# Optimization experiments

Measured on AMD Instinct MI355X. Metric: run time of the kernel, lower is better.

## Reference

```python
import jax, jax.numpy as jnp
import numpy as np

DIM = 64
HEADS = 8
WIN = (8, 8)  # window_num


def setup_inputs() -> dict:
    key = jax.random.key(0)
    ks = jax.random.split(key, 6)
    b, c, H, W = 16, DIM, 256, 256
    n = WIN[0] * WIN[1]
    x = jax.random.normal(ks[0], (b, c, H, W), dtype=jnp.float32)
    w_qkv = jax.random.normal(ks[1], (3 * c, c), dtype=jnp.float32) * (1.0 / np.sqrt(c))
    w_dw = jax.random.normal(ks[2], (3 * c, 1, 3, 3), dtype=jnp.float32) * (1.0 / 3.0)
    w_proj = jax.random.normal(ks[3], (c, c), dtype=jnp.float32) * (1.0 / np.sqrt(c))
    b_proj = jnp.zeros((c,), dtype=jnp.float32)
    # trunc_normal_(std=1) approximated by clipped normal for the reference baseline
    pos_emb = jnp.clip(jax.random.normal(ks[4], (1, HEADS, n, n), dtype=jnp.float32), -2.0, 2.0)
    return {"x": x, "w_qkv": w_qkv, "w_dw": w_dw, "w_proj": w_proj,
            "b_proj": b_proj, "pos_emb": pos_emb}


def _to_window_tokens(t, n0, n1, heads):
    # t: [b, c, n0*b0, n1*b1] -> [b, heads, n0*n1, (b0*b1*c)//heads]
    b, c, H, W = t.shape
    b0, b1 = H // n0, W // n1
    t = t.reshape(b, c, n0, b0, n1, b1)
    t = t.transpose(0, 2, 4, 3, 5, 1)            # b n0 n1 b0 b1 c
    t = t.reshape(b, n0 * n1, b0 * b1 * c)       # b n (b0 b1 c)
    d = (b0 * b1 * c) // heads
    return t.reshape(b, n0 * n1, heads, d).transpose(0, 2, 1, 3)  # b h n d


def _from_window_tokens(t, n0, n1, b0, b1, c):
    # t: [b, heads, n, d] -> [b, c, n0*b0, n1*b1]
    b = t.shape[0]
    t = t.transpose(0, 2, 1, 3).reshape(b, n0 * n1, b0 * b1 * c)  # b n (h d)
    t = t.reshape(b, n0, n1, b0, b1, c)
    t = t.transpose(0, 5, 1, 3, 2, 4)            # b c n0 b0 n1 b1
    return t.reshape(b, c, n0 * b0, n1 * b1)


def reference(x, w_qkv, w_dw, w_proj, b_proj, pos_emb):
    b, c, H, W = x.shape
    n0, n1 = WIN
    b0, b1 = H // n0, W // n1
    # 1x1 pointwise qkv projection (no bias)
    qkv = jnp.einsum('bchw,oc->bohw', x, w_qkv)
    # 3x3 depthwise conv, padding=1, groups=3c, no bias
    qkv = jax.lax.conv_general_dilated(
        qkv, w_dw, window_strides=(1, 1), padding=((1, 1), (1, 1)),
        feature_group_count=3 * c,
        dimension_numbers=('NCHW', 'OIHW', 'NCHW'))
    q, k, v = jnp.split(qkv, 3, axis=1)
    q = _to_window_tokens(q, n0, n1, HEADS)
    k = _to_window_tokens(k, n0, n1, HEADS)
    v = _to_window_tokens(v, n0, n1, HEADS)
    head_dim = b0 * b1 * c / HEADS
    scale = head_dim ** (-0.5)
    sim = jnp.einsum('bhid,bhjd->bhij', q * scale, k) + pos_emb
    attn = jax.nn.softmax(sim, axis=-1)
    out = jnp.einsum('bhij,bhjd->bhid', attn, v)
    out = _from_window_tokens(out, n0, n1, b0, b1, c)
    # 1x1 projection with bias
    out = jnp.einsum('bchw,oc->bohw', out, w_proj) + b_proj[None, :, None, None]
    return out
```

## Files before the change

### kernel.cpp

```cpp
#include <hip/hip_runtime.h>
#include <hip/hip_bf16.h>

typedef __hip_bfloat16 bf16;
typedef unsigned int u32;
typedef __attribute__((ext_vector_type(8))) short bf16x8;
typedef __attribute__((ext_vector_type(4))) float f32x4;

#define HWSZ 65536u

__device__ __forceinline__ float b2f_lo(u32 w){ return __uint_as_float(w << 16); }
__device__ __forceinline__ float b2f_hi(u32 w){ return __uint_as_float(w & 0xffff0000u); }
__device__ __forceinline__ float b2f(bf16 v){ return __bfloat162float(v); }
__device__ __forceinline__ bf16 f2b(float v){ return __float2bfloat16(v); }

__device__ __forceinline__ u32 f2bbits(float f){
  u32 x = __float_as_uint(f);
  return ((x + 0x7fffu + ((x >> 16) & 1u)) >> 16) & 0xffffu;
}

__device__ __forceinline__ void unpack8(uint4 v, float* f){
  f[0]=b2f_lo(v.x); f[1]=b2f_hi(v.x);
  f[2]=b2f_lo(v.y); f[3]=b2f_hi(v.y);
  f[4]=b2f_lo(v.z); f[5]=b2f_hi(v.z);
  f[6]=b2f_lo(v.w); f[7]=b2f_hi(v.w);
}

union ABu { u32 u[4]; bf16x8 v; uint4 q; };

__global__ __launch_bounds__(256) void k12_fused(
    const float* __restrict__ x, const float* __restrict__ wq,
    const float* __restrict__ wdw, bf16* __restrict__ tok){
  __shared__ uint4 xs[8 * 192];
  __shared__ unsigned short qs[192 * 68];
  int t = threadIdx.x;
  int lane = t & 63, w = t >> 6;
  int r16 = lane & 15, g4 = lane >> 4;

  u32 n = blockIdx.x;
  u32 bid = (n & 7u) * 1024u + (n >> 3);
  u32 xt = bid & 31u, yt = (bid >> 5) & 15u, b = bid >> 9;
  int y0 = (int)yt * 16, x0 = (int)xt * 8;

  const float* xb = x + (size_t)b * 64 * HWSZ;

  bf16x8 af[3][2];
  #pragma unroll
  for (int g = 0; g < 3; g++){
    int och = g * 64 + w * 16 + r16;
    #pragma unroll
    for (int kt = 0; kt < 2; kt++){
      const float* wr = wq + och * 64 + kt * 32 + g4 * 8;
      ABu pk;
      #pragma unroll
      for (int j = 0; j < 4; j++)
        pk.u[j] = f2bbits(wr[2 * j]) | (f2bbits(wr[2 * j + 1]) << 16);
      af[g][kt] = pk.v;
    }
  }

  for (int u = t; u < 288; u += 256){
    int jh = u & 1, rr = (u >> 1) % 18, c8 = u / 36;
    int yy = y0 - 1 + rr;
    float va[4][10];
    if ((u32)yy < 256u){
      #pragma unroll
      for (int jc = 0; jc < 4; jc++){
        const float* p = xb + (size_t)(c8 * 8 + jh * 4 + jc) * HWSZ + ((size_t)yy << 8);
        float4 A  = *(const float4*)(p + x0);
        float4 Bq = *(const float4*)(p + x0 + 4);
        va[jc][0] = (x0 > 0) ? p[x0 - 1] : 0.f;
        va[jc][1] = A.x;  va[jc][2] = A.y;  va[jc][3] = A.z;  va[jc][4] = A.w;
        va[jc][5] = Bq.x; va[jc][6] = Bq.y; va[jc][7] = Bq.z; va[jc][8] = Bq.w;
        va[jc][9] = (x0 + 8 < 256) ? p[x0 + 8] : 0.f;
      }
    } else {
      #pragma unroll
      for (int jc = 0; jc < 4; jc++)
        #pragma unroll
        for (int e = 0; e < 10; e++) va[jc][e] = 0.f;
    }
    #pragma unroll
    for (int e = 0; e < 10; e++){
      u32 w0 = f2bbits(va[0][e]) | (f2bbits(va[1][e]) << 16);
      u32 w1 = f2bbits(va[2][e]) | (f2bbits(va[3][e]) << 16);
      int a16 = c8 * 192 + rr * 10 + e;
      a16 = (a16 & ~7) | ((a16 ^ (a16 >> 3)) & 7);
      ((uint2*)&xs[a16])[jh] = make_uint2(w0, w1);
    }
  }
  if (t < 96){
    int c8 = t / 12, px = 180 + (t % 12);
    int a16 = c8 * 192 + px;
    a16 = (a16 & ~7) | ((a16 ^ (a16 >> 3)) & 7);
    xs[a16] = make_uint4(0u, 0u, 0u, 0u);
  }

  int cth = t & 63, rq = w;
  int h = (int)(yt & 1u) * 4 + rq;
  u32 win = (yt >> 1) * 8u + (xt >> 2);

  for (int g = 0; g < 3; g++){
    __syncthreads();
    #pragma unroll
    for (int nt = 0; nt < 12; nt++){
      f32x4 acc = (f32x4){0.f, 0.f, 0.f, 0.f};
      #pragma unroll
      for (int kt = 0; kt < 2; kt++){
        int a16 = (kt * 4 + g4) * 192 + nt * 16 + r16;
        a16 = (a16 & ~7) | ((a16 ^ (a16 >> 3)) & 7);
        uint4 uq = xs[a16];
        acc = __builtin_amdgcn_mfma_f32_16x16x32_bf16(
            af[g][kt], *reinterpret_cast<bf16x8*>(&uq), acc, 0, 0, 0);
      }
      int px = nt * 16 + r16;
      u32 lo = f2bbits(acc[0]) | (f2bbits(acc[1]) << 16);
      u32 hi = f2bbits(acc[2]) | (f2bbits(acc[3]) << 16);
      *(uint2*)&qs[px * 68 + w * 16 + g4 * 4] = make_uint2(lo, hi);
    }
    __syncthreads();

    const float* wg = wdw + ((size_t)g * 64 + cth) * 9;
    float d0=wg[0],d1=wg[1],d2=wg[2],d3=wg[3],d4=wg[4],d5=wg[5],d6=wg[6],d7=wg[7],d8=wg[8];
    bf16* op = tok + (((((size_t)g * 16 + b) * 8 + h) * 64 + win) * 8192)
             + (size_t)(xt & 3u) * 512 + cth;
    float rbf[3][10];
    #define QLD(s, R) do{ _Pragma("unroll") for (int _cr = 0; _cr < 10; _cr++) \
      rbf[s][_cr] = __uint_as_float(((u32)qs[((R) * 10 + _cr) * 68 + cth]) << 16); }while(0)
    QLD(0, rq * 4 + 0);
    QLD(1, rq * 4 + 1);
    QLD(2, rq * 4 + 2);
    #pragma unroll
    for (int rr2 = 0; rr2 < 4; rr2++){
      const int sT = rr2 % 3, sM = (rr2 + 1) % 3, sB = (rr2 + 2) % 3;
      #pragma unroll
      for (int co = 0; co < 8; co++){
        float o = rbf[sT][co]*d0 + rbf[sT][co+1]*d1 + rbf[sT][co+2]*d2
                + rbf[sM][co]*d3 + rbf[sM][co+1]*d4 + rbf[sM][co+2]*d5
                + rbf[sB][co]*d6 + rbf[sB][co+1]*d7 + rbf[sB][co+2]*d8;
        op[(size_t)rr2 * 2048 + co * 64] = f2b(o);
      }
      if (rr2 < 3) QLD(sT, rq * 4 + rr2 + 3);
    }
    #undef QLD
  }
}

__global__ __launch_bounds__(256) void k3_sim(
    const bf16* __restrict__ tok, float* __restrict__ sim4){
  __shared__ short qs[64 * 72];
  __shared__ short ks[64 * 72];
  int t = threadIdx.x;
  int lane = t & 63, w = t >> 6;
  int r16 = lane & 15, g4 = lane >> 4;
  u32 bid = blockIdx.x;
  u32 part = bid & 3u, h = (bid >> 2) & 7u, b = bid >> 5;
  const bf16* qb = tok + ((size_t)(((0 * 16 + b) * 8 + h) * 64)) * 8192 + part * 2048;
  const bf16* kb = tok + ((size_t)(((1 * 16 + b) * 8 + h) * 64)) * 8192 + part * 2048;

  int stok = t >> 2, soct = t & 3;

  f32x4 acc[4];
  #pragma unroll
  for (int jt = 0; jt < 4; jt++) acc[jt] = (f32x4){0.f,0.f,0.f,0.f};

  for (int s = 0; s < 32; s++){
    int d0 = s * 64;
    __syncthreads();
    {
      uint4 q0 = *(const uint4*)(qb + (size_t)stok * 8192 + d0 + soct * 8);
      uint4 q1 = *(const uint4*)(qb + (size_t)stok * 8192 + d0 + soct * 8 + 32);
      uint4 k0 = *(const uint4*)(kb + (size_t)stok * 8192 + d0 + soct * 8);
      uint4 k1 = *(const uint4*)(kb + (size_t)stok * 8192 + d0 + soct * 8 + 32);
      *(uint4*)&qs[stok * 72 + soct * 8]      = q0;
      *(uint4*)&qs[stok * 72 + soct * 8 + 32] = q1;
      *(uint4*)&ks[stok * 72 + soct * 8]      = k0;
      *(uint4*)&ks[stok * 72 + soct * 8 + 32] = k1;
    }
    __syncthreads();
    #pragma unroll
    for (int kt = 0; kt < 2; kt++){
      bf16x8 a = *(const bf16x8*)&qs[(w * 16 + r16) * 72 + kt * 32 + g4 * 8];
      #pragma unroll
      for (int jt = 0; jt < 4; jt++){
        bf16x8 bb = *(const bf16x8*)&ks[(jt * 16 + r16) * 72 + kt * 32 + g4 * 8];
        acc[jt] = __builtin_amdgcn_mfma_f32_16x16x32_bf16(a, bb, acc[jt], 0, 0, 0);
      }
    }
  }

  float* sp = sim4 + ((((size_t)part * 16 + b) * 8 + h) * 64) * 64;
  #pragma unroll
  for (int jt = 0; jt < 4; jt++)
    #pragma unroll
    for (int r = 0; r < 4; r++)
      sp[(w * 16 + g4 * 4 + r) * 64 + jt * 16 + r16] = acc[jt][r];
}

__global__ __launch_bounds__(64) void k4_softmax(
    const float* __restrict__ sim4, const float* __restrict__ pos, float* __restrict__ attn){
  int j = threadIdx.x;
  u32 bid = blockIdx.x;
  u32 i = bid & 63u, h = (bid >> 6) & 7u, b = bid >> 9;
  size_t o = (((size_t)b * 8 + h) * 64 + i) * 64 + j;
  const size_t pstride = (size_t)16 * 8 * 64 * 64;
  float s = sim4[o] + sim4[o + pstride] + sim4[o + 2 * pstride] + sim4[o + 3 * pstride];
  s = s * 0.011048543456039806f + pos[(((size_t)h * 64) + i) * 64 + j];
  float m = s;
  #pragma unroll
  for (int off = 32; off; off >>= 1) m = fmaxf(m, __shfl_xor(m, off));
  float e = __expf(s - m);
  float sum = e;
  #pragma unroll
  for (int off = 32; off; off >>= 1) sum += __shfl_xor(sum, off);
  attn[o] = e / sum;
}

__global__ __launch_bounds__(256) void k5_av(
    const bf16* __restrict__ tok, const float* __restrict__ attn, bf16* __restrict__ otok){
  __shared__ short vt[4][64 * 72];
  int t = threadIdx.x;
  int lane = t & 63, w = t >> 6;
  int r16 = lane & 15, g4 = lane >> 4;
  u32 bid = blockIdx.x;
  u32 q = bid & 3u, h = (bid >> 2) & 7u, b = bid >> 5;
  const bf16* vb = tok + ((size_t)(((2 * 16 + b) * 8 + h) * 64)) * 8192;
  const float* ab = attn + (((size_t)b * 8 + h) * 64) * 64;
  bf16* ob = otok + (((size_t)b * 8 + h) * 64) * 8192;

  bf16x8 af[4][2];
  #pragma unroll
  for (int it = 0; it < 4; it++)
    #pragma unroll
    for (int kt = 0; kt < 2; kt++){
      const float* ar = ab + (it * 16 + r16) * 64 + kt * 32 + g4 * 8;
      ABu pk;
      #pragma unroll
      for (int j = 0; j < 4; j++)
        pk.u[j] = f2bbits(ar[2 * j]) | (f2bbits(ar[2 * j + 1]) << 16);
      af[it][kt] = pk.v;
    }

  short* vtw = vt[w];
  for (int s = 0; s < 8; s++){
    int d0 = (int)q * 2048 + s * 256 + w * 64;
    uint4 ld[8];
    const bf16* vp = vb + (size_t)lane * 8192 + d0;
    #pragma unroll
    for (int u = 0; u < 8; u++) ld[u] = *(const uint4*)(vp + u * 8);
    #pragma unroll
    for (int u = 0; u < 8; u++){
      const u32* wd = (const u32*)&ld[u];
      #pragma unroll
      for (int e = 0; e < 4; e++){
        int d = u * 8 + e * 2;
        vtw[d * 72 + lane]       = (short)(wd[e] & 0xffffu);
        vtw[(d + 1) * 72 + lane] = (short)(wd[e] >> 16);
      }
    }
    #pragma unroll
    for (int dt = 0; dt < 4; dt++){
      bf16x8 b0 = *(const bf16x8*)&vtw[(dt * 16 + r16) * 72 + 0 * 32 + g4 * 8];
      bf16x8 b1 = *(const bf16x8*)&vtw[(dt * 16 + r16) * 72 + 1 * 32 + g4 * 8];
      #pragma unroll
      for (int it = 0; it < 4; it++){
        f32x4 acc = (f32x4){0.f,0.f,0.f,0.f};
        acc = __builtin_amdgcn_mfma_f32_16x16x32_bf16(af[it][0], b0, acc, 0, 0, 0);
        acc = __builtin_amdgcn_mfma_f32_16x16x32_bf16(af[it][1], b1, acc, 0, 0, 0);
        #pragma unroll
        for (int r = 0; r < 4; r++)
          ob[(size_t)(it * 16 + g4 * 4 + r) * 8192 + d0 + dt * 16 + r16] = f2b(acc[r]);
      }
    }
  }
}

__global__ __launch_bounds__(256) void k6_mfma(
    const bf16* __restrict__ otok, const float* __restrict__ wp,
    const float* __restrict__ bp, float* __restrict__ out){
  __shared__ uint4 xs[1024];
  int t = threadIdx.x;
  int lane = t & 63, w = t >> 6;
  u32 pix0 = blockIdx.x * 128u;
  u32 b = pix0 >> 16, hw0 = pix0 & 65535u;
  int y = (int)(hw0 >> 8);
  int p0 = y & 31, h = p0 >> 2, prow = (p0 & 3) * 2048;
  int iy = (y >> 5) << 3;

  {
    int pix = t & 127, half = t >> 7;
    int xx = (int)(hw0 & 255u) + pix;
    int i = iy + (xx >> 5), p1 = xx & 31;
    const bf16* ip = otok + ((((size_t)b * 8 + h) * 64 + i)) * 8192 + prow + p1 * 64;
    #pragma unroll
    for (int g = 0; g < 4; g++){
      int c8 = half * 4 + g;
      xs[c8 * 128 + pix] = *(const uint4*)(ip + c8 * 8);
    }
  }

  int r16 = lane & 15, g4 = lane >> 4;
  bf16x8 af[2];
  int och = w * 16 + r16;
  #pragma unroll
  for (int kt = 0; kt < 2; kt++){
    const float* wr = wp + och * 64 + kt * 32 + g4 * 8;
    ABu pk;
    #pragma unroll
    for (int j = 0; j < 4; j++)
      pk.u[j] = f2bbits(wr[2 * j]) | (f2bbits(wr[2 * j + 1]) << 16);
    af[kt] = pk.v;
  }
  float bias[4];
  #pragma unroll
  for (int r = 0; r < 4; r++) bias[r] = bp[w * 16 + g4 * 4 + r];
  __syncthreads();

  f32x4 acc[8];
  #pragma unroll
  for (int pt = 0; pt < 8; pt++) acc[pt] = (f32x4){bias[0], bias[1], bias[2], bias[3]};

  #pragma unroll
  for (int pt = 0; pt < 8; pt++){
    uint4 u0 = xs[(0 * 4 + g4) * 128 + pt * 16 + r16];
    uint4 u1 = xs[(1 * 4 + g4) * 128 + pt * 16 + r16];
    bf16x8 b0 = *reinterpret_cast<bf16x8*>(&u0);
    bf16x8 b1 = *reinterpret_cast<bf16x8*>(&u1);
    acc[pt] = __builtin_amdgcn_mfma_f32_16x16x32_bf16(af[0], b0, acc[pt], 0, 0, 0);
    acc[pt] = __builtin_amdgcn_mfma_f32_16x16x32_bf16(af[1], b1, acc[pt], 0, 0, 0);
  }

  float* op = out + (size_t)b * 64 * HWSZ + hw0;
  int ochb = w * 16 + g4 * 4;
  #pragma unroll
  for (int pt = 0; pt < 8; pt++)
    #pragma unroll
    for (int r = 0; r < 4; r++)
      op[(size_t)(ochb + r) * HWSZ + pt * 16 + r16] = acc[pt][r];
}

extern "C" void kernel_launch(void* const* d_in, const int* in_sizes, int n_in,
                              void* d_out, int out_size, void* d_ws, size_t ws_size,
                              hipStream_t stream){
  const float* x   = (const float*)d_in[0];
  const float* wq  = (const float*)d_in[1];
  const float* wdw = (const float*)d_in[2];
  const float* wp  = (const float*)d_in[3];
  const float* bp  = (const float*)d_in[4];
  const float* pos = (const float*)d_in[5];
  float* out = (float*)d_out;
  (void)in_sizes; (void)n_in; (void)out_size; (void)ws_size;

  char* ws = (char*)d_ws;
  bf16*  tok  = (bf16*)(ws + 402653184u);
  bf16*  otok = (bf16*)ws;
  float* sim4 = (float*)(ws + 134217728u);
  float* attn = (float*)(ws + 142606336u);

  k12_fused<<<dim3(8192), dim3(256), 0, stream>>>(x, wq, wdw, tok);
  k3_sim<<<dim3(512),   dim3(256), 0, stream>>>(tok, sim4);
  k4_softmax<<<dim3(8192), dim3(64), 0, stream>>>(sim4, pos, attn);
  k5_av<<<dim3(512),  dim3(256), 0, stream>>>(tok, attn, otok);
  k6_mfma<<<dim3(8192), dim3(256), 0, stream>>>(otok, wp, bp, out);
}
```

Before: 524.7 us.

## Double k12 block to 512 threads and split work across more waves

The fused qkv-projection plus depthwise-conv kernel now runs 512 threads per block instead of 256. Each wave handles half the MFMA pixel tiles and two output rows instead of four, and the staging load is spread over more threads. Weight fragments are loaded per group inside the loop instead of all up front, which lowers register pressure so that launch_bounds(512,6) can be met. The aim is more latency hiding and occupancy, at the cost of redundant weight loads and extra halo row reads in the depthwise stage.

```diff
diff --git a/kernel.cpp b/kernel.cpp
--- a/kernel.cpp
+++ b/kernel.cpp
@@ -27,7 +27,11 @@
 
 union ABu { u32 u[4]; bf16x8 v; uint4 q; };
 
-__global__ __launch_bounds__(256) void k12_fused(
+__device__ __forceinline__ int xsw(int c8, int px){
+  return c8 * 192 + ((px & ~7) | ((px ^ c8) & 7));
+}
+
+__global__ __launch_bounds__(512, 6) void k12_fused(
     const float* __restrict__ x, const float* __restrict__ wq,
     const float* __restrict__ wdw, bf16* __restrict__ tok){
   __shared__ uint4 xs[8 * 192];
@@ -43,29 +47,14 @@
 
   const float* xb = x + (size_t)b * 64 * HWSZ;
 
-  bf16x8 af[3][2];
-  #pragma unroll
-  for (int g = 0; g < 3; g++){
-    int och = g * 64 + w * 16 + r16;
-    #pragma unroll
-    for (int kt = 0; kt < 2; kt++){
-      const float* wr = wq + och * 64 + kt * 32 + g4 * 8;
-      ABu pk;
-      #pragma unroll
-      for (int j = 0; j < 4; j++)
-        pk.u[j] = f2bbits(wr[2 * j]) | (f2bbits(wr[2 * j + 1]) << 16);
-      af[g][kt] = pk.v;
-    }
-  }
-
-  for (int u = t; u < 288; u += 256){
-    int jh = u & 1, rr = (u >> 1) % 18, c8 = u / 36;
+  for (int u = t; u < 576; u += 512){
+    int jq = u & 3, rr = (u >> 2) % 18, c8 = u / 72;
     int yy = y0 - 1 + rr;
-    float va[4][10];
+    float va[2][10];
     if ((u32)yy < 256u){
       #pragma unroll
-      for (int jc = 0; jc < 4; jc++){
-        const float* p = xb + (size_t)(c8 * 8 + jh * 4 + jc) * HWSZ + ((size_t)yy << 8);
+      for (int jc = 0; jc < 2; jc++){
+        const float* p = xb + (size_t)(c8 * 8 + jq * 2 + jc) * HWSZ + ((size_t)yy << 8);
         float4 A  = *(const float4*)(p + x0);
         float4 Bq = *(const float4*)(p + x0 + 4);
         va[jc][0] = (x0 > 0) ? p[x0 - 1] : 0.f;
@@ -75,73 +64,81 @@
       }
     } else {
       #pragma unroll
-      for (int jc = 0; jc < 4; jc++)
+      for (int jc = 0; jc < 2; jc++)
         #pragma unroll
         for (int e = 0; e < 10; e++) va[jc][e] = 0.f;
     }
     #pragma unroll
     for (int e = 0; e < 10; e++){
-      u32 w0 = f2bbits(va[0][e]) | (f2bbits(va[1][e]) << 16);
-      u32 w1 = f2bbits(va[2][e]) | (f2bbits(va[3][e]) << 16);
-      int a16 = c8 * 192 + rr * 10 + e;
-      a16 = (a16 & ~7) | ((a16 ^ (a16 >> 3)) & 7);
-      ((uint2*)&xs[a16])[jh] = make_uint2(w0, w1);
+      u32 wv = f2bbits(va[0][e]) | (f2bbits(va[1][e]) << 16);
+      ((u32*)&xs[xsw(c8, rr * 10 + e)])[jq] = wv;
     }
   }
   if (t < 96){
     int c8 = t / 12, px = 180 + (t % 12);
-    int a16 = c8 * 192 + px;
-    a16 = (a16 & ~7) | ((a16 ^ (a16 >> 3)) & 7);
-    xs[a16] = make_uint4(0u, 0u, 0u, 0u);
-  }
-
-  int cth = t & 63, rq = w;
-  int h = (int)(yt & 1u) * 4 + rq;
+    xs[xsw(c8, px)] = make_uint4(0u, 0u, 0u, 0u);
+  }
+
+  int cth = lane, rp = w;
+  int ot = w & 3, nh = w >> 2;
   u32 win = (yt >> 1) * 8u + (xt >> 2);
 
   for (int g = 0; g < 3; g++){
     __syncthreads();
-    #pragma unroll
-    for (int nt = 0; nt < 12; nt++){
+    bf16x8 af[2];
+    {
+      int och = g * 64 + ot * 16 + r16;
+      #pragma unroll
+      for (int kt = 0; kt < 2; kt++){
+        const float* wr = wq + och * 64 + kt * 32 + g4 * 8;
+        ABu pk;
+        #pragma unroll
+        for (int j = 0; j < 4; j++)
+          pk.u[j] = f2bbits(wr[2 * j]) | (f2bbits(wr[2 * j + 1]) << 16);
+        af[kt] = pk.v;
+      }
+    }
+    #pragma unroll
+    for (int nt2 = 0; nt2 < 6; nt2++){
+      int nt = nh * 6 + nt2;
       f32x4 acc = (f32x4){0.f, 0.f, 0.f, 0.f};
       #pragma unroll
       for (int kt = 0; kt < 2; kt++){
-        int a16 = (kt * 4 + g4) * 192 + nt * 16 + r16;
-        a16 = (a16 & ~7) | ((a16 ^ (a16 >> 3)) & 7);
-        uint4 uq = xs[a16];
+        uint4 uq = xs[xsw(kt * 4 + g4, nt * 16 + r16)];
         acc = __builtin_amdgcn_mfma_f32_16x16x32_bf16(
-            af[g][kt], *reinterpret_cast<bf16x8*>(&uq), acc, 0, 0, 0);
+            af[kt], *reinterpret_cast<bf16x8*>(&uq), acc, 0, 0, 0);
       }
       int px = nt * 16 + r16;
       u32 lo = f2bbits(acc[0]) | (f2bbits(acc[1]) << 16);
       u32 hi = f2bbits(acc[2]) | (f2bbits(acc[3]) << 16);
-      *(uint2*)&qs[px * 68 + w * 16 + g4 * 4] = make_uint2(lo, hi);
+      *(uint2*)&qs[px * 68 + ot * 16 + g4 * 4] = make_uint2(lo, hi);
     }
     __syncthreads();
 
     const float* wg = wdw + ((size_t)g * 64 + cth) * 9;
     float d0=wg[0],d1=wg[1],d2=wg[2],d3=wg[3],d4=wg[4],d5=wg[5],d6=wg[6],d7=wg[7],d8=wg[8];
-    bf16* op = tok + (((((size_t)g * 16 + b) * 8 + h) * 64 + win) * 8192)
-             + (size_t)(xt & 3u) * 512 + cth;
-    float rbf[3][10];
+    float rbf[4][10];
     #define QLD(s, R) do{ _Pragma("unroll") for (int _cr = 0; _cr < 10; _cr++) \
       rbf[s][_cr] = __uint_as_float(((u32)qs[((R) * 10 + _cr) * 68 + cth]) << 16); }while(0)
-    QLD(0, rq * 4 + 0);
-    QLD(1, rq * 4 + 1);
-    QLD(2, rq * 4 + 2);
-    #pragma unroll
-    for (int rr2 = 0; rr2 < 4; rr2++){
-      const int sT = rr2 % 3, sM = (rr2 + 1) % 3, sB = (rr2 + 2) % 3;
+    QLD(0, rp * 2 + 0);
+    QLD(1, rp * 2 + 1);
+    QLD(2, rp * 2 + 2);
+    QLD(3, rp * 2 + 3);
+    #undef QLD
+    #pragma unroll
+    for (int rr2 = 0; rr2 < 2; rr2++){
+      int r = rp * 2 + rr2;
+      int h = (int)(yt & 1u) * 4 + (r >> 2);
+      bf16* op = tok + (((((size_t)g * 16 + b) * 8 + h) * 64 + win) * 8192)
+               + (size_t)(r & 3) * 2048 + (size_t)(xt & 3u) * 512 + cth;
       #pragma unroll
       for (int co = 0; co < 8; co++){
-        float o = rbf[sT][co]*d0 + rbf[sT][co+1]*d1 + rbf[sT][co+2]*d2
-                + rbf[sM][co]*d3 + rbf[sM][co+1]*d4 + rbf[sM][co+2]*d5
-                + rbf[sB][co]*d6 + rbf[sB][co+1]*d7 + rbf[sB][co+2]*d8;
-        op[(size_t)rr2 * 2048 + co * 64] = f2b(o);
-      }
-      if (rr2 < 3) QLD(sT, rq * 4 + rr2 + 3);
-    }
-    #undef QLD
+        float o = rbf[rr2][co]    * d0 + rbf[rr2][co + 1]    * d1 + rbf[rr2][co + 2]    * d2
+                + rbf[rr2 + 1][co]* d3 + rbf[rr2 + 1][co + 1]* d4 + rbf[rr2 + 1][co + 2]* d5
+                + rbf[rr2 + 2][co]* d6 + rbf[rr2 + 2][co + 1]* d7 + rbf[rr2 + 2][co + 2]* d8;
+        op[co * 64] = f2b(o);
+      }
+    }
   }
 }
 
@@ -356,7 +353,7 @@
   float* sim4 = (float*)(ws + 134217728u);
   float* attn = (float*)(ws + 142606336u);
 
-  k12_fused<<<dim3(8192), dim3(256), 0, stream>>>(x, wq, wdw, tok);
+  k12_fused<<<dim3(8192), dim3(512), 0, stream>>>(x, wq, wdw, tok);
   k3_sim<<<dim3(512),   dim3(256), 0, stream>>>(tok, sim4);
   k4_softmax<<<dim3(8192), dim3(64), 0, stream>>>(sim4, pos, attn);
   k5_av<<<dim3(512),  dim3(256), 0, stream>>>(tok, attn, otok);
```

Measured after the change: 549.6 us. 4.7% more time.

## Fuse softmax into attention-value kernel and swizzle LDS with channel group

Applied to the files above, without the earlier changes.

Removes the standalone softmax kernel. The AV kernel now reads the four partial sim buffers and the positional bias, then does the row softmax in registers with cross-lane shuffles before packing bf16 MFMA operands. This saves one launch and the attn round trip through global memory. Each of the 4 q-blocks per (b,h) now recomputes the same softmax, which is redundant work. Separately, the k12 LDS swizzle now XORs in the channel-group index to cut bank conflicts, and the qkv weight fragments are loaded per group to lower register pressure.

```diff
diff --git a/kernel.cpp b/kernel.cpp
--- a/kernel.cpp
+++ b/kernel.cpp
@@ -18,14 +18,11 @@
   return ((x + 0x7fffu + ((x >> 16) & 1u)) >> 16) & 0xffffu;
 }
 
-__device__ __forceinline__ void unpack8(uint4 v, float* f){
-  f[0]=b2f_lo(v.x); f[1]=b2f_hi(v.x);
-  f[2]=b2f_lo(v.y); f[3]=b2f_hi(v.y);
-  f[4]=b2f_lo(v.z); f[5]=b2f_hi(v.z);
-  f[6]=b2f_lo(v.w); f[7]=b2f_hi(v.w);
-}
-
 union ABu { u32 u[4]; bf16x8 v; uint4 q; };
+
+__device__ __forceinline__ int xsw(int c8, int px){
+  return c8 * 192 + ((px & ~7) | ((px ^ (px >> 3) ^ c8) & 7));
+}
 
 __global__ __launch_bounds__(256) void k12_fused(
     const float* __restrict__ x, const float* __restrict__ wq,
@@ -43,21 +40,6 @@
 
   const float* xb = x + (size_t)b * 64 * HWSZ;
 
-  bf16x8 af[3][2];
-  #pragma unroll
-  for (int g = 0; g < 3; g++){
-    int och = g * 64 + w * 16 + r16;
-    #pragma unroll
-    for (int kt = 0; kt < 2; kt++){
-      const float* wr = wq + och * 64 + kt * 32 + g4 * 8;
-      ABu pk;
-      #pragma unroll
-      for (int j = 0; j < 4; j++)
-        pk.u[j] = f2bbits(wr[2 * j]) | (f2bbits(wr[2 * j + 1]) << 16);
-      af[g][kt] = pk.v;
-    }
-  }
-
   for (int u = t; u < 288; u += 256){
     int jh = u & 1, rr = (u >> 1) % 18, c8 = u / 36;
     int yy = y0 - 1 + rr;
@@ -83,16 +65,12 @@
     for (int e = 0; e < 10; e++){
       u32 w0 = f2bbits(va[0][e]) | (f2bbits(va[1][e]) << 16);
       u32 w1 = f2bbits(va[2][e]) | (f2bbits(va[3][e]) << 16);
-      int a16 = c8 * 192 + rr * 10 + e;
-      a16 = (a16 & ~7) | ((a16 ^ (a16 >> 3)) & 7);
-      ((uint2*)&xs[a16])[jh] = make_uint2(w0, w1);
+      ((uint2*)&xs[xsw(c8, rr * 10 + e)])[jh] = make_uint2(w0, w1);
     }
   }
   if (t < 96){
     int c8 = t / 12, px = 180 + (t % 12);
-    int a16 = c8 * 192 + px;
-    a16 = (a16 & ~7) | ((a16 ^ (a16 >> 3)) & 7);
-    xs[a16] = make_uint4(0u, 0u, 0u, 0u);
+    xs[xsw(c8, px)] = make_uint4(0u, 0u, 0u, 0u);
   }
 
   int cth = t & 63, rq = w;
@@ -101,16 +79,27 @@
 
   for (int g = 0; g < 3; g++){
     __syncthreads();
+    bf16x8 af[2];
+    {
+      int och = g * 64 + w * 16 + r16;
+      #pragma unroll
+      for (int kt = 0; kt < 2; kt++){
+        const float* wr = wq + och * 64 + kt * 32 + g4 * 8;
+        ABu pk;
+        #pragma unroll
+        for (int j = 0; j < 4; j++)
+          pk.u[j] = f2bbits(wr[2 * j]) | (f2bbits(wr[2 * j + 1]) << 16);
+        af[kt] = pk.v;
+      }
+    }
     #pragma unroll
     for (int nt = 0; nt < 12; nt++){
       f32x4 acc = (f32x4){0.f, 0.f, 0.f, 0.f};
       #pragma unroll
       for (int kt = 0; kt < 2; kt++){
-        int a16 = (kt * 4 + g4) * 192 + nt * 16 + r16;
-        a16 = (a16 & ~7) | ((a16 ^ (a16 >> 3)) & 7);
-        uint4 uq = xs[a16];
+        uint4 uq = xs[xsw(kt * 4 + g4, nt * 16 + r16)];
         acc = __builtin_amdgcn_mfma_f32_16x16x32_bf16(
-            af[g][kt], *reinterpret_cast<bf16x8*>(&uq), acc, 0, 0, 0);
+            af[kt], *reinterpret_cast<bf16x8*>(&uq), acc, 0, 0, 0);
       }
       int px = nt * 16 + r16;
       u32 lo = f2bbits(acc[0]) | (f2bbits(acc[1]) << 16);
@@ -196,27 +185,9 @@
       sp[(w * 16 + g4 * 4 + r) * 64 + jt * 16 + r16] = acc[jt][r];
 }
 
-__global__ __launch_bounds__(64) void k4_softmax(
-    const float* __restrict__ sim4, const float* __restrict__ pos, float* __restrict__ attn){
-  int j = threadIdx.x;
-  u32 bid = blockIdx.x;
-  u32 i = bid & 63u, h = (bid >> 6) & 7u, b = bid >> 9;
-  size_t o = (((size_t)b * 8 + h) * 64 + i) * 64 + j;
-  const size_t pstride = (size_t)16 * 8 * 64 * 64;
-  float s = sim4[o] + sim4[o + pstride] + sim4[o + 2 * pstride] + sim4[o + 3 * pstride];
-  s = s * 0.011048543456039806f + pos[(((size_t)h * 64) + i) * 64 + j];
-  float m = s;
-  #pragma unroll
-  for (int off = 32; off; off >>= 1) m = fmaxf(m, __shfl_xor(m, off));
-  float e = __expf(s - m);
-  float sum = e;
-  #pragma unroll
-  for (int off = 32; off; off >>= 1) sum += __shfl_xor(sum, off);
-  attn[o] = e / sum;
-}
-
 __global__ __launch_bounds__(256) void k5_av(
-    const bf16* __restrict__ tok, const float* __restrict__ attn, bf16* __restrict__ otok){
+    const bf16* __restrict__ tok, const float* __restrict__ sim4,
+    const float* __restrict__ pos, bf16* __restrict__ otok){
   __shared__ short vt[4][64 * 72];
   int t = threadIdx.x;
   int lane = t & 63, w = t >> 6;
@@ -224,21 +195,59 @@
   u32 bid = blockIdx.x;
   u32 q = bid & 3u, h = (bid >> 2) & 7u, b = bid >> 5;
   const bf16* vb = tok + ((size_t)(((2 * 16 + b) * 8 + h) * 64)) * 8192;
-  const float* ab = attn + (((size_t)b * 8 + h) * 64) * 64;
   bf16* ob = otok + (((size_t)b * 8 + h) * 64) * 8192;
 
+  const float* s0 = sim4 + (((size_t)b * 8 + h) * 64) * 64;
+  const size_t pstr = (size_t)16 * 8 * 64 * 64;
+  const float* pb = pos + ((size_t)h * 64) * 64;
+  const float SC = 0.011048543456039806f;
+
   bf16x8 af[4][2];
   #pragma unroll
-  for (int it = 0; it < 4; it++)
+  for (int it = 0; it < 4; it++){
+    int row = it * 16 + r16;
+    const float* rp = s0 + (size_t)row * 64;
+    float ev[2][8];
     #pragma unroll
     for (int kt = 0; kt < 2; kt++){
-      const float* ar = ab + (it * 16 + r16) * 64 + kt * 32 + g4 * 8;
+      int jb = kt * 32 + g4 * 8;
+      #pragma unroll
+      for (int hq = 0; hq < 2; hq++){
+        float4 a0 = *(const float4*)(rp + jb + hq * 4);
+        float4 a1 = *(const float4*)(rp + pstr + jb + hq * 4);
+        float4 a2 = *(const float4*)(rp + 2 * pstr + jb + hq * 4);
+        float4 a3 = *(const float4*)(rp + 3 * pstr + jb + hq * 4);
+        float4 pe = *(const float4*)(pb + (size_t)row * 64 + jb + hq * 4);
+        ev[kt][hq * 4 + 0] = (a0.x + a1.x + a2.x + a3.x) * SC + pe.x;
+        ev[kt][hq * 4 + 1] = (a0.y + a1.y + a2.y + a3.y) * SC + pe.y;
+        ev[kt][hq * 4 + 2] = (a0.z + a1.z + a2.z + a3.z) * SC + pe.z;
+        ev[kt][hq * 4 + 3] = (a0.w + a1.w + a2.w + a3.w) * SC + pe.w;
+      }
+    }
+    float m = ev[0][0];
+    #pragma unroll
+    for (int kt = 0; kt < 2; kt++)
+      #pragma unroll
+      for (int j = 0; j < 8; j++) m = fmaxf(m, ev[kt][j]);
+    m = fmaxf(m, __shfl_xor(m, 16));
+    m = fmaxf(m, __shfl_xor(m, 32));
+    float sum = 0.f;
+    #pragma unroll
+    for (int kt = 0; kt < 2; kt++)
+      #pragma unroll
+      for (int j = 0; j < 8; j++){ ev[kt][j] = __expf(ev[kt][j] - m); sum += ev[kt][j]; }
+    sum += __shfl_xor(sum, 16);
+    sum += __shfl_xor(sum, 32);
+    float inv = 1.f / sum;
+    #pragma unroll
+    for (int kt = 0; kt < 2; kt++){
       ABu pk;
       #pragma unroll
       for (int j = 0; j < 4; j++)
-        pk.u[j] = f2bbits(ar[2 * j]) | (f2bbits(ar[2 * j + 1]) << 16);
+        pk.u[j] = f2bbits(ev[kt][2 * j] * inv) | (f2bbits(ev[kt][2 * j + 1] * inv) << 16);
       af[it][kt] = pk.v;
     }
+  }
 
   short* vtw = vt[w];
   for (int s = 0; s < 8; s++){
@@ -354,11 +363,9 @@
   bf16*  tok  = (bf16*)(ws + 402653184u);
   bf16*  otok = (bf16*)ws;
   float* sim4 = (float*)(ws + 134217728u);
-  float* attn = (float*)(ws + 142606336u);
 
   k12_fused<<<dim3(8192), dim3(256), 0, stream>>>(x, wq, wdw, tok);
   k3_sim<<<dim3(512),   dim3(256), 0, stream>>>(tok, sim4);
-  k4_softmax<<<dim3(8192), dim3(64), 0, stream>>>(sim4, pos, attn);
-  k5_av<<<dim3(512),  dim3(256), 0, stream>>>(tok, attn, otok);
+  k5_av<<<dim3(512),  dim3(256), 0, stream>>>(tok, sim4, pos, otok);
   k6_mfma<<<dim3(8192), dim3(256), 0, stream>>>(otok, wp, bp, out);
 }
```

New measurement: 565.7 us. 1.08x slower.
